# Performance work log

Hardware: AMD Instinct MI355X
Metric: run time of the kernel (lower is better)

The kernel has to match this reference:

```python
import jax, jax.numpy as jnp
import numpy as np

N, D_IN, H, L, K, Q = 131072, 384, 256, 32, 512, 4


def _lin_init(key, fan_in, fan_out):
    s = 1.0 / np.sqrt(fan_in)
    kw, kb = jax.random.split(key)
    w = jax.random.uniform(kw, (fan_in, fan_out), minval=-s, maxval=s, dtype=jnp.float32)
    b = jax.random.uniform(kb, (fan_out,), minval=-s, maxval=s, dtype=jnp.float32)
    return w, b


def setup_inputs() -> dict:
    key = jax.random.key(0)
    ks = jax.random.split(key, 8)
    enc_w1, enc_b1 = _lin_init(ks[1], D_IN, H)
    enc_w2, enc_b2 = _lin_init(ks[2], H, H)
    enc_w3, enc_b3 = _lin_init(ks[3], H, L)
    dec_w1, dec_b1 = _lin_init(ks[4], L, H)
    dec_w2, dec_b2 = _lin_init(ks[5], H, H)
    dec_w3, dec_b3 = _lin_init(ks[6], H, D_IN)
    codebooks = jax.random.normal(ks[7], (Q, K, L), dtype=jnp.float32) * 0.02
    x = jax.random.normal(ks[0], (N, D_IN), dtype=jnp.float32)
    return dict(x=x,
                enc_w1=enc_w1, enc_b1=enc_b1, enc_w2=enc_w2, enc_b2=enc_b2,
                enc_w3=enc_w3, enc_b3=enc_b3,
                dec_w1=dec_w1, dec_b1=dec_b1, dec_w2=dec_w2, dec_b2=dec_b2,
                dec_w3=dec_w3, dec_b3=dec_b3,
                codebooks=codebooks)


def _encoder(x, w1, b1, w2, b2, w3, b3):
    h = jax.nn.relu(x @ w1 + b1)
    h = jax.nn.relu(h @ w2 + b2)
    return h @ w3 + b3


def _decoder(z, w1, b1, w2, b2, w3, b3):
    h = jax.nn.relu(z @ w1 + b1)
    h = jax.nn.relu(h @ w2 + b2)
    return h @ w3 + b3


def _residual_vq(z, codebooks):
    """Residual VQ: Q stages of nearest-codeword lookup on the running residual.
    Returns (z_quantized with straight-through, indices [N,Q], commitment loss)."""
    residual = z
    quant_sum = jnp.zeros_like(z)
    indices = []
    commit = jnp.float32(0.0)
    for q in range(codebooks.shape[0]):  # small fixed loop over quantizer stages
        cb = codebooks[q]  # [K, L]
        # squared L2 distances [N, K] via expansion (cdist + argmin)
        d = (jnp.sum(residual * residual, axis=-1, keepdims=True)
             - 2.0 * residual @ cb.T
             + jnp.sum(cb * cb, axis=-1))
        idx = jnp.argmin(d, axis=-1)          # [N]
        qv = cb[idx]                          # gather [N, L]
        commit = commit + jnp.mean((jax.lax.stop_gradient(qv) - residual) ** 2)
        quant_sum = quant_sum + qv
        residual = residual - jax.lax.stop_gradient(qv)
        indices.append(idx)
    # straight-through estimator
    z_q = z + jax.lax.stop_gradient(quant_sum - z)
    return z_q, jnp.stack(indices, axis=-1), commit


def reference(x, enc_w1, enc_b1, enc_w2, enc_b2, enc_w3, enc_b3,
              dec_w1, dec_b1, dec_w2, dec_b2, dec_w3, dec_b3, codebooks):
    z = _encoder(x, enc_w1, enc_b1, enc_w2, enc_b2, enc_w3, enc_b3)
    z_q, indices, commit = _residual_vq(z, codebooks)
    x_recon = _decoder(z_q, dec_w1, dec_b1, dec_w2, dec_b2, dec_w3, dec_b3)
    return x_recon, indices, commit
```

## Files before the change

### kernel.cpp

```cpp
#include <hip/hip_runtime.h>
#include <hip/hip_bf16.h>
#include <math.h>


#define N_ROWS 131072
#define D_IN   384
#define H_DIM  256
#define L_DIM  32
#define K_CB   512
#define Q_ST   4
#define VQ_RPB 128
#define NPART  (N_ROWS / VQ_RPB)

typedef __attribute__((ext_vector_type(8))) short short8v;
typedef __attribute__((ext_vector_type(4))) float f32x4;

__device__ __forceinline__ ushort f2bf(float v)
{
    __hip_bfloat16 b = __float2bfloat16(v);
    return *reinterpret_cast<ushort*>(&b);
}

__device__ __forceinline__ float np_sumsq32(const float* __restrict__ v)
{
    #pragma clang fp contract(off)
    float s0 = v[0]*v[0], s1 = v[1]*v[1], s2 = v[2]*v[2], s3 = v[3]*v[3];
    float s4 = v[4]*v[4], s5 = v[5]*v[5], s6 = v[6]*v[6], s7 = v[7]*v[7];
    s0 = s0 + v[8]*v[8];   s1 = s1 + v[9]*v[9];   s2 = s2 + v[10]*v[10]; s3 = s3 + v[11]*v[11];
    s4 = s4 + v[12]*v[12]; s5 = s5 + v[13]*v[13]; s6 = s6 + v[14]*v[14]; s7 = s7 + v[15]*v[15];
    s0 = s0 + v[16]*v[16]; s1 = s1 + v[17]*v[17]; s2 = s2 + v[18]*v[18]; s3 = s3 + v[19]*v[19];
    s4 = s4 + v[20]*v[20]; s5 = s5 + v[21]*v[21]; s6 = s6 + v[22]*v[22]; s7 = s7 + v[23]*v[23];
    s0 = s0 + v[24]*v[24]; s1 = s1 + v[25]*v[25]; s2 = s2 + v[26]*v[26]; s3 = s3 + v[27]*v[27];
    s4 = s4 + v[28]*v[28]; s5 = s5 + v[29]*v[29]; s6 = s6 + v[30]*v[30]; s7 = s7 + v[31]*v[31];
    return ((s0 + s1) + (s2 + s3)) + ((s4 + s5) + (s6 + s7));
}

template<bool RELU>
__global__ __launch_bounds__(256, 2)
void gemm_bias(const float* __restrict__ A, const float* __restrict__ B,
               const float* __restrict__ bias, float* __restrict__ C,
               int K)
{
    #pragma clang fp contract(off)
    __shared__ float As2[32][133];
    __shared__ float Bs[32][256];
    const int t  = threadIdx.x;
    const int tc = t & 15;
    const int tr = t >> 4;
    const size_t row0 = (size_t)blockIdx.x * 128;

    float acc[8][16];
    #pragma unroll
    for (int i = 0; i < 8; ++i)
        #pragma unroll
        for (int j = 0; j < 16; ++j) acc[i][j] = 0.f;

    const int ar = t >> 3, ak = (t & 7) << 2;
    const int brow = t >> 6, bcol = (t & 63) << 2;

    for (int k0 = 0; k0 < K; k0 += 32) {
        #pragma unroll
        for (int i = 0; i < 4; ++i) {
            int r = ar + (i << 5);
            float4 v = *reinterpret_cast<const float4*>(A + (row0 + r) * (size_t)K + k0 + ak);
            As2[ak + 0][r] = v.x; As2[ak + 1][r] = v.y;
            As2[ak + 2][r] = v.z; As2[ak + 3][r] = v.w;
        }
        #pragma unroll
        for (int i = 0; i < 8; ++i) {
            int rb = brow + (i << 2);
            float4 v = *reinterpret_cast<const float4*>(B + (size_t)(k0 + rb) * H_DIM + bcol);
            *reinterpret_cast<float4*>(&Bs[rb][bcol]) = v;
        }
        __syncthreads();
        #pragma unroll
        for (int k = 0; k < 32; ++k) {
            float a[8], b[16];
            *reinterpret_cast<float4*>(&a[0]) = *reinterpret_cast<const float4*>(&As2[k][tr << 3]);
            *reinterpret_cast<float4*>(&a[4]) = *reinterpret_cast<const float4*>(&As2[k][(tr << 3) + 4]);
            #pragma unroll
            for (int g = 0; g < 4; ++g)
                *reinterpret_cast<float4*>(&b[g << 2]) =
                    *reinterpret_cast<const float4*>(&Bs[k][(g << 6) + (tc << 2)]);
            #pragma unroll
            for (int i = 0; i < 8; ++i)
                #pragma unroll
                for (int j = 0; j < 16; ++j) acc[i][j] = fmaf(a[i], b[j], acc[i][j]);
        }
        __syncthreads();
    }

    #pragma unroll
    for (int i = 0; i < 8; ++i) {
        size_t r = row0 + (tr << 3) + i;
        #pragma unroll
        for (int g = 0; g < 4; ++g) {
            int c = (g << 6) + (tc << 2);
            float v[4];
            #pragma unroll
            for (int j = 0; j < 4; ++j) {
                float u = acc[i][(g << 2) + j] + bias[c + j];
                if (RELU) u = fmaxf(u, 0.0f);
                v[j] = u;
            }
            *reinterpret_cast<float4*>(C + r * H_DIM + c) = *reinterpret_cast<float4*>(&v[0]);
        }
    }
}

__global__ __launch_bounds__(256)
void gemm_z(const float* __restrict__ A, const float* __restrict__ W,
            const float* __restrict__ bv, float* __restrict__ Z)
{
    #pragma clang fp contract(off)
    __shared__ float As2[32][133];
    __shared__ float Ws[32][36];
    const int t = threadIdx.x;
    const int cgz = t & 7, rgz = t >> 3;
    const size_t row0 = (size_t)blockIdx.x * 128;

    float acc[4][4];
    #pragma unroll
    for (int i = 0; i < 4; ++i)
        #pragma unroll
        for (int j = 0; j < 4; ++j) acc[i][j] = 0.f;

    const int ar = t >> 3, ak = (t & 7) << 2;
    for (int k0 = 0; k0 < H_DIM; k0 += 32) {
        #pragma unroll
        for (int i = 0; i < 4; ++i) {
            int r = ar + (i << 5);
            float4 v = *reinterpret_cast<const float4*>(A + (row0 + r) * (size_t)H_DIM + k0 + ak);
            As2[ak + 0][r] = v.x; As2[ak + 1][r] = v.y;
            As2[ak + 2][r] = v.z; As2[ak + 3][r] = v.w;
        }
        {
            int kr = t >> 3, cc = (t & 7) << 2;
            float4 v = *reinterpret_cast<const float4*>(W + (size_t)(k0 + kr) * L_DIM + cc);
            *reinterpret_cast<float4*>(&Ws[kr][cc]) = v;
        }
        __syncthreads();
        #pragma unroll
        for (int k = 0; k < 32; ++k) {
            float a[4], w[4];
            *reinterpret_cast<float4*>(&a[0]) = *reinterpret_cast<const float4*>(&As2[k][rgz << 2]);
            *reinterpret_cast<float4*>(&w[0]) = *reinterpret_cast<const float4*>(&Ws[k][cgz << 2]);
            #pragma unroll
            for (int i = 0; i < 4; ++i)
                #pragma unroll
                for (int j = 0; j < 4; ++j) acc[i][j] = fmaf(a[i], w[j], acc[i][j]);
        }
        __syncthreads();
    }
    #pragma unroll
    for (int i = 0; i < 4; ++i) {
        size_t row = row0 + (rgz << 2) + i;
        float v[4];
        #pragma unroll
        for (int j = 0; j < 4; ++j) v[j] = acc[i][j] + bv[(cgz << 2) + j];
        *reinterpret_cast<float4*>(Z + row * L_DIM + (cgz << 2)) = *reinterpret_cast<float4*>(&v[0]);
    }
}

__global__ __launch_bounds__(256)
void cnorm_kernel(const float* __restrict__ cbs, float* __restrict__ cnorm)
{
    #pragma clang fp contract(off)
    int g = blockIdx.x * 256 + threadIdx.x;
    const float* c = cbs + (size_t)g * L_DIM;
    float cl[L_DIM];
    #pragma unroll
    for (int l = 0; l < L_DIM; ++l) cl[l] = c[l];
    cnorm[g] = np_sumsq32(cl);
}

__global__ __launch_bounds__(256)
void prep_wt(const float* __restrict__ W, ushort* __restrict__ Wt, int K, int N)
{
    int g = blockIdx.x * 256 + threadIdx.x;
    if (g >= K * N) return;
    int n = g / K, k = g - n * K;
    Wt[g] = f2bf(W[(size_t)k * N + n]);
}

__global__ __launch_bounds__(256)
void vq9_kernel(const float* __restrict__ zbuf, const float* __restrict__ cbs,
                const float* __restrict__ cnorm_g, ushort* __restrict__ zqb,
                float* __restrict__ idxOut, double* __restrict__ commitPart,
                int rowBase)
{
    #pragma clang fp contract(off)
    __shared__ float  cbL[K_CB * L_DIM];
    __shared__ float  cnL[K_CB];
    __shared__ float  sd0[4][64], sd1[4][64];
    __shared__ int    si0[4][64], si1[4][64];
    __shared__ double sred[256];

    const int t = threadIdx.x;
    const int w = t >> 6;
    const int l = t & 63;
    const size_t lrow0 = (size_t)blockIdx.x * VQ_RPB + l;
    const size_t lrow1 = lrow0 + 64;
    const size_t grow0 = (size_t)rowBase + lrow0;
    const size_t grow1 = (size_t)rowBase + lrow1;
    const int c0 = w << 7;

    float r0[L_DIM], r1[L_DIM];
    {
        const float4* zp0 = reinterpret_cast<const float4*>(zbuf + lrow0 * L_DIM);
        const float4* zp1 = reinterpret_cast<const float4*>(zbuf + lrow1 * L_DIM);
        #pragma unroll
        for (int j = 0; j < 8; ++j) {
            float4 a = zp0[j], b = zp1[j];
            r0[4*j+0]=a.x; r0[4*j+1]=a.y; r0[4*j+2]=a.z; r0[4*j+3]=a.w;
            r1[4*j+0]=b.x; r1[4*j+1]=b.y; r1[4*j+2]=b.z; r1[4*j+3]=b.w;
        }
    }

    int bidx0[Q_ST], bidx1[Q_ST];
    double cAcc = 0.0;

    #pragma unroll 1
    for (int q = 0; q < Q_ST; ++q) {
        __syncthreads();
        {
            const float4* src = reinterpret_cast<const float4*>(cbs + (size_t)q * K_CB * L_DIM);
            float4* dst = reinterpret_cast<float4*>(cbL);
            #pragma unroll
            for (int i = 0; i < 16; ++i) dst[t + (i << 8)] = src[t + (i << 8)];
            cnL[t]       = cnorm_g[q * K_CB + t];
            cnL[t + 256] = cnorm_g[q * K_CB + t + 256];
        }
        __syncthreads();

        float rr0 = np_sumsq32(r0);
        float rr1 = np_sumsq32(r1);
        float bd0 = __builtin_inff(), bd1 = __builtin_inff();
        int   bi0 = c0, bi1 = c0;

        #pragma unroll 1
        for (int cc = 0; cc < 128; cc += 2) {
            const int c = c0 + cc;
            const float4* w0 = reinterpret_cast<const float4*>(cbL + (c << 5));
            const float4* w1 = w0 + 8;
            float a00 = 0.f, a01 = 0.f, a10 = 0.f, a11 = 0.f;
            #pragma unroll
            for (int j = 0; j < 8; ++j) {
                float4 u = w0[j], v = w1[j];
                a00 = fmaf(r0[4*j+0], u.x, a00);  a01 = fmaf(r0[4*j+0], v.x, a01);
                a10 = fmaf(r1[4*j+0], u.x, a10);  a11 = fmaf(r1[4*j+0], v.x, a11);
                a00 = fmaf(r0[4*j+1], u.y, a00);  a01 = fmaf(r0[4*j+1], v.y, a01);
                a10 = fmaf(r1[4*j+1], u.y, a10);  a11 = fmaf(r1[4*j+1], v.y, a11);
                a00 = fmaf(r0[4*j+2], u.z, a00);  a01 = fmaf(r0[4*j+2], v.z, a01);
                a10 = fmaf(r1[4*j+2], u.z, a10);  a11 = fmaf(r1[4*j+2], v.z, a11);
                a00 = fmaf(r0[4*j+3], u.w, a00);  a01 = fmaf(r0[4*j+3], v.w, a01);
                a10 = fmaf(r1[4*j+3], u.w, a10);  a11 = fmaf(r1[4*j+3], v.w, a11);
            }
            float cn0 = cnL[c], cn1 = cnL[c + 1];
            float d00 = (rr0 - 2.0f * a00) + cn0;
            float d01 = (rr0 - 2.0f * a01) + cn1;
            float d10 = (rr1 - 2.0f * a10) + cn0;
            float d11 = (rr1 - 2.0f * a11) + cn1;
            if (d00 < bd0) { bd0 = d00; bi0 = c; }
            if (d01 < bd0) { bd0 = d01; bi0 = c + 1; }
            if (d10 < bd1) { bd1 = d10; bi1 = c; }
            if (d11 < bd1) { bd1 = d11; bi1 = c + 1; }
        }

        sd0[w][l] = bd0; si0[w][l] = bi0;
        sd1[w][l] = bd1; si1[w][l] = bi1;
        __syncthreads();

        float g0 = sd0[0][l]; int gi0 = si0[0][l];
        float g1 = sd1[0][l]; int gi1 = si1[0][l];
        #pragma unroll
        for (int ww = 1; ww < 4; ++ww) {
            float od = sd0[ww][l]; int oi = si0[ww][l];
            if (od < g0 || (od == g0 && oi < gi0)) { g0 = od; gi0 = oi; }
            od = sd1[ww][l]; oi = si1[ww][l];
            if (od < g1 || (od == g1 && oi < gi1)) { g1 = od; gi1 = oi; }
        }
        bidx0[q] = gi0;
        bidx1[q] = gi1;

        {
            const float4* p0 = reinterpret_cast<const float4*>(cbL + (gi0 << 5));
            const float4* p1 = reinterpret_cast<const float4*>(cbL + (gi1 << 5));
            float cs0 = 0.f, cs1 = 0.f;
            #pragma unroll
            for (int j = 0; j < 8; ++j) {
                float4 v0 = p0[j], v1 = p1[j];
                float df;
                df = v0.x - r0[4*j+0]; cs0 = fmaf(df, df, cs0); r0[4*j+0] = r0[4*j+0] - v0.x;
                df = v0.y - r0[4*j+1]; cs0 = fmaf(df, df, cs0); r0[4*j+1] = r0[4*j+1] - v0.y;
                df = v0.z - r0[4*j+2]; cs0 = fmaf(df, df, cs0); r0[4*j+2] = r0[4*j+2] - v0.z;
                df = v0.w - r0[4*j+3]; cs0 = fmaf(df, df, cs0); r0[4*j+3] = r0[4*j+3] - v0.w;
                df = v1.x - r1[4*j+0]; cs1 = fmaf(df, df, cs1); r1[4*j+0] = r1[4*j+0] - v1.x;
                df = v1.y - r1[4*j+1]; cs1 = fmaf(df, df, cs1); r1[4*j+1] = r1[4*j+1] - v1.y;
                df = v1.z - r1[4*j+2]; cs1 = fmaf(df, df, cs1); r1[4*j+2] = r1[4*j+2] - v1.z;
                df = v1.w - r1[4*j+3]; cs1 = fmaf(df, df, cs1); r1[4*j+3] = r1[4*j+3] - v1.w;
            }
            if (w == 0) { cAcc += (double)cs0; cAcc += (double)cs1; }
        }
    }

    if (w == 0) {
        float4 iv0 = make_float4((float)bidx0[0], (float)bidx0[1], (float)bidx0[2], (float)bidx0[3]);
        float4 iv1 = make_float4((float)bidx1[0], (float)bidx1[1], (float)bidx1[2], (float)bidx1[3]);
        *reinterpret_cast<float4*>(idxOut + grow0 * Q_ST) = iv0;
        *reinterpret_cast<float4*>(idxOut + grow1 * Q_ST) = iv1;

        const float4* zp0 = reinterpret_cast<const float4*>(zbuf + lrow0 * L_DIM);
        const float4* zp1 = reinterpret_cast<const float4*>(zbuf + lrow1 * L_DIM);
        ushort zq0[L_DIM], zq1[L_DIM];
        #pragma unroll
        for (int j = 0; j < 8; ++j) {
            float4 a = zp0[j], b = zp1[j];
            zq0[4*j+0] = f2bf(a.x - r0[4*j+0]);
            zq0[4*j+1] = f2bf(a.y - r0[4*j+1]);
            zq0[4*j+2] = f2bf(a.z - r0[4*j+2]);
            zq0[4*j+3] = f2bf(a.w - r0[4*j+3]);
            zq1[4*j+0] = f2bf(b.x - r1[4*j+0]);
            zq1[4*j+1] = f2bf(b.y - r1[4*j+1]);
            zq1[4*j+2] = f2bf(b.z - r1[4*j+2]);
            zq1[4*j+3] = f2bf(b.w - r1[4*j+3]);
        }
        uint4* o0 = reinterpret_cast<uint4*>(zqb + lrow0 * L_DIM);
        uint4* o1 = reinterpret_cast<uint4*>(zqb + lrow1 * L_DIM);
        const uint4* s0 = reinterpret_cast<const uint4*>(zq0);
        const uint4* s1 = reinterpret_cast<const uint4*>(zq1);
        #pragma unroll
        for (int j = 0; j < 4; ++j) { o0[j] = s0[j]; o1[j] = s1[j]; }
    }

    sred[t] = (w == 0) ? cAcc : 0.0;
    __syncthreads();
    for (int s = 128; s > 0; s >>= 1) {
        if (t < s) sred[t] += sred[t + s];
        __syncthreads();
    }
    if (t == 0) commitPart[rowBase / VQ_RPB + blockIdx.x] = sred[0];
}

template<bool RELU, bool OUTBF16>
__global__ __launch_bounds__(256)
void mfma_gemm(const ushort* __restrict__ A, const ushort* __restrict__ Bt,
               const float* __restrict__ bias, void* __restrict__ Cout,
               int K, int Nout)
{
    __shared__ ushort As[128][40];
    __shared__ ushort Bs[128][40];
    const int t    = threadIdx.x;
    const int lane = t & 63;
    const int wid  = t >> 6;
    const int wr = wid >> 1, wc = wid & 1;
    const size_t row0 = (size_t)blockIdx.x * 128;
    const int    col0 = blockIdx.y * 128;

    f32x4 acc[4][4] = {};
    const int srow = t >> 1;
    const int sh   = (t & 1) << 4;

    for (int k0 = 0; k0 < K; k0 += 32) {
        {
            const ushort* ap = A + (row0 + srow) * (size_t)K + k0 + sh;
            uint4 v0 = *reinterpret_cast<const uint4*>(ap);
            uint4 v1 = *reinterpret_cast<const uint4*>(ap + 8);
            *reinterpret_cast<uint4*>(&As[srow][sh])     = v0;
            *reinterpret_cast<uint4*>(&As[srow][sh + 8]) = v1;
            const ushort* bp = Bt + (size_t)(col0 + srow) * K + k0 + sh;
            uint4 w0 = *reinterpret_cast<const uint4*>(bp);
            uint4 w1 = *reinterpret_cast<const uint4*>(bp + 8);
            *reinterpret_cast<uint4*>(&Bs[srow][sh])     = w0;
            *reinterpret_cast<uint4*>(&Bs[srow][sh + 8]) = w1;
        }
        __syncthreads();
        const int l15 = lane & 15, lk = (lane >> 4) << 3;
        short8v af[4], bf[4];
        #pragma unroll
        for (int f = 0; f < 4; ++f) {
            af[f] = *reinterpret_cast<const short8v*>(&As[(wr << 6) + (f << 4) + l15][lk]);
            bf[f] = *reinterpret_cast<const short8v*>(&Bs[(wc << 6) + (f << 4) + l15][lk]);
        }
        #pragma unroll
        for (int i = 0; i < 4; ++i)
            #pragma unroll
            for (int j = 0; j < 4; ++j)
                acc[i][j] = __builtin_amdgcn_mfma_f32_16x16x32_bf16(af[i], bf[j], acc[i][j], 0, 0, 0);
        __syncthreads();
    }

    const int l15 = lane & 15, lr4 = (lane >> 4) << 2;
    #pragma unroll
    for (int i = 0; i < 4; ++i) {
        #pragma unroll
        for (int j = 0; j < 4; ++j) {
            int col = col0 + (wc << 6) + (j << 4) + l15;
            float bv = bias[col];
            #pragma unroll
            for (int rj = 0; rj < 4; ++rj) {
                size_t row = row0 + (wr << 6) + (i << 4) + lr4 + rj;
                float v = acc[i][j][rj] + bv;
                if (RELU) v = fmaxf(v, 0.f);
                if (OUTBF16)
                    reinterpret_cast<ushort*>(Cout)[row * Nout + col] = f2bf(v);
                else
                    reinterpret_cast<float*>(Cout)[row * Nout + col] = v;
            }
        }
    }
}

__global__ __launch_bounds__(256)
void commit_finalize(const double* __restrict__ commitPart, float* __restrict__ outCommit)
{
    __shared__ double sred[256];
    const int t = threadIdx.x;
    double s = 0.0;
    for (int i = t; i < NPART; i += 256) s += commitPart[i];
    sred[t] = s;
    __syncthreads();
    for (int st = 128; st > 0; st >>= 1) {
        if (t < st) sred[t] += sred[t + st];
        __syncthreads();
    }
    if (t == 0)
        outCommit[0] = (float)(sred[0] / ((double)N_ROWS * (double)L_DIM));
}

extern "C" void kernel_launch(void* const* d_in, const int* in_sizes, int n_in,
                              void* d_out, int out_size, void* d_ws, size_t ws_size,
                              hipStream_t stream)
{
    const float* x      = (const float*)d_in[0];
    const float* enc_w1 = (const float*)d_in[1];
    const float* enc_b1 = (const float*)d_in[2];
    const float* enc_w2 = (const float*)d_in[3];
    const float* enc_b2 = (const float*)d_in[4];
    const float* enc_w3 = (const float*)d_in[5];
    const float* enc_b3 = (const float*)d_in[6];
    const float* dec_w1 = (const float*)d_in[7];
    const float* dec_b1 = (const float*)d_in[8];
    const float* dec_w2 = (const float*)d_in[9];
    const float* dec_b2 = (const float*)d_in[10];
    const float* dec_w3 = (const float*)d_in[11];
    const float* dec_b3 = (const float*)d_in[12];
    const float* cbs    = (const float*)d_in[13];

    float* out       = (float*)d_out;
    float* xrec      = out;
    float* idxOut    = out + (size_t)N_ROWS * D_IN;
    float* commitOut = idxOut + (size_t)N_ROWS * Q_ST;

    char*   wsb        = (char*)d_ws;
    float*  cnorm      = (float*)wsb;
    double* commitPart = (double*)(wsb + 8192);
    ushort* w1t        = (ushort*)(wsb + 16384);
    ushort* w2t        = (ushort*)(wsb + 32768);
    ushort* w3t        = (ushort*)(wsb + 163840);
    char*   bufs       = wsb + 360448;

    size_t availB = (ws_size > 360448) ? ws_size - 360448 : 0;
    long long chunk = (long long)(availB / 3264);
    chunk = (chunk / 256) * 256;
    if (chunk > N_ROWS) chunk = N_ROWS;
    if (chunk < 256) chunk = 256;

    float*  zbuf = (float*)bufs;
    float*  bufA = zbuf + (size_t)chunk * L_DIM;
    float*  bufB = bufA + (size_t)chunk * H_DIM;
    ushort* zqb  = (ushort*)(bufB + (size_t)chunk * H_DIM);
    ushort* h1b  = zqb + (size_t)chunk * L_DIM;
    ushort* h2b  = h1b + (size_t)chunk * H_DIM;

    cnorm_kernel<<<8, 256, 0, stream>>>(cbs, cnorm);
    prep_wt<<<(L_DIM  * H_DIM + 255) / 256, 256, 0, stream>>>(dec_w1, w1t, L_DIM, H_DIM);
    prep_wt<<<(H_DIM * H_DIM + 255) / 256, 256, 0, stream>>>(dec_w2, w2t, H_DIM, H_DIM);
    prep_wt<<<(H_DIM * D_IN + 255) / 256, 256, 0, stream>>>(dec_w3, w3t, H_DIM, D_IN);

    for (long long ro = 0; ro < N_ROWS; ro += chunk) {
        long long R = N_ROWS - ro;
        if (R > chunk) R = chunk;
        unsigned g1 = (unsigned)(R / 128);
        dim3 g2(g1, 2);
        dim3 g3(g1, 3);
        gemm_bias<true><<<g1, 256, 0, stream>>>(x + ro * D_IN, enc_w1, enc_b1, bufA, D_IN);
        gemm_bias<true><<<g1, 256, 0, stream>>>(bufA, enc_w2, enc_b2, bufB, H_DIM);
        gemm_z<<<g1, 256, 0, stream>>>(bufB, enc_w3, enc_b3, zbuf);
        vq9_kernel<<<(unsigned)(R / VQ_RPB), 256, 0, stream>>>(zbuf, cbs, cnorm, zqb,
                                                               idxOut, commitPart, (int)ro);
        mfma_gemm<true,  true ><<<g2, 256, 0, stream>>>(zqb, w1t, dec_b1, h1b, L_DIM, H_DIM);
        mfma_gemm<true,  true ><<<g2, 256, 0, stream>>>(h1b, w2t, dec_b2, h2b, H_DIM, H_DIM);
        mfma_gemm<false, false><<<g3, 256, 0, stream>>>(h2b, w3t, dec_b3, xrec + ro * D_IN, H_DIM, D_IN);
    }

    commit_finalize<<<1, 256, 0, stream>>>(commitPart, commitOut);
}
```

Measured before the change: 919.3 us.

## Restructure encoder fp32 GEMM to read B via wave-uniform scalar loads

Replaces the encoder fp32 GEMM's shared-memory B tile with wave-uniform reads straight from global memory. Each wave owns 64 output columns and each lane owns two rows, so B values can be fetched with scalar loads and broadcast, cutting LDS traffic and one staging step. The cost is 128 accumulators per thread, which raises register pressure and lowers occupancy, and B reads now rely on the scalar cache instead of LDS. The A tile is still staged transposed in LDS.

```diff
diff --git a/kernel.cpp b/kernel.cpp
--- a/kernel.cpp
+++ b/kernel.cpp
@@ -36,27 +36,24 @@
 }
 
 template<bool RELU>
-__global__ __launch_bounds__(256, 2)
-void gemm_bias(const float* __restrict__ A, const float* __restrict__ B,
-               const float* __restrict__ bias, float* __restrict__ C,
-               int K)
+__global__ __launch_bounds__(256)
+void gemm_sb(const float* __restrict__ A, const float* __restrict__ B,
+             const float* __restrict__ bias, float* __restrict__ C,
+             int K)
 {
     #pragma clang fp contract(off)
     __shared__ float As2[32][133];
-    __shared__ float Bs[32][256];
-    const int t  = threadIdx.x;
-    const int tc = t & 15;
-    const int tr = t >> 4;
+    const int t = threadIdx.x;
+    const int l = t & 63;
+    const int w = __builtin_amdgcn_readfirstlane(t >> 6);
+    const int cbase = w << 6;
     const size_t row0 = (size_t)blockIdx.x * 128;
 
-    float acc[8][16];
-    #pragma unroll
-    for (int i = 0; i < 8; ++i)
-        #pragma unroll
-        for (int j = 0; j < 16; ++j) acc[i][j] = 0.f;
+    float acc0[64], acc1[64];
+    #pragma unroll
+    for (int j = 0; j < 64; ++j) { acc0[j] = 0.f; acc1[j] = 0.f; }
 
     const int ar = t >> 3, ak = (t & 7) << 2;
-    const int brow = t >> 6, bcol = (t & 63) << 2;
 
     for (int k0 = 0; k0 < K; k0 += 32) {
         #pragma unroll
@@ -66,45 +63,37 @@
             As2[ak + 0][r] = v.x; As2[ak + 1][r] = v.y;
             As2[ak + 2][r] = v.z; As2[ak + 3][r] = v.w;
         }
-        #pragma unroll
-        for (int i = 0; i < 8; ++i) {
-            int rb = brow + (i << 2);
-            float4 v = *reinterpret_cast<const float4*>(B + (size_t)(k0 + rb) * H_DIM + bcol);
-            *reinterpret_cast<float4*>(&Bs[rb][bcol]) = v;
-        }
-        __syncthreads();
-        #pragma unroll
+        __syncthreads();
+        #pragma unroll 2
         for (int k = 0; k < 32; ++k) {
-            float a[8], b[16];
-            *reinterpret_cast<float4*>(&a[0]) = *reinterpret_cast<const float4*>(&As2[k][tr << 3]);
-            *reinterpret_cast<float4*>(&a[4]) = *reinterpret_cast<const float4*>(&As2[k][(tr << 3) + 4]);
-            #pragma unroll
-            for (int g = 0; g < 4; ++g)
-                *reinterpret_cast<float4*>(&b[g << 2]) =
-                    *reinterpret_cast<const float4*>(&Bs[k][(g << 6) + (tc << 2)]);
-            #pragma unroll
-            for (int i = 0; i < 8; ++i)
-                #pragma unroll
-                for (int j = 0; j < 16; ++j) acc[i][j] = fmaf(a[i], b[j], acc[i][j]);
-        }
-        __syncthreads();
-    }
-
-    #pragma unroll
-    for (int i = 0; i < 8; ++i) {
-        size_t r = row0 + (tr << 3) + i;
-        #pragma unroll
-        for (int g = 0; g < 4; ++g) {
-            int c = (g << 6) + (tc << 2);
-            float v[4];
-            #pragma unroll
-            for (int j = 0; j < 4; ++j) {
-                float u = acc[i][(g << 2) + j] + bias[c + j];
-                if (RELU) u = fmaxf(u, 0.0f);
-                v[j] = u;
+            float a0 = As2[k][l];
+            float a1 = As2[k][l + 64];
+            const float* __restrict__ Brow = B + (size_t)(k0 + k) * H_DIM + cbase;
+            #pragma unroll
+            for (int j = 0; j < 64; ++j) {
+                float bv = Brow[j];
+                acc0[j] = fmaf(a0, bv, acc0[j]);
+                acc1[j] = fmaf(a1, bv, acc1[j]);
             }
-            *reinterpret_cast<float4*>(C + r * H_DIM + c) = *reinterpret_cast<float4*>(&v[0]);
-        }
+        }
+        __syncthreads();
+    }
+
+    float* C0 = C + (row0 + l) * (size_t)H_DIM + cbase;
+    float* C1 = C + (row0 + l + 64) * (size_t)H_DIM + cbase;
+    #pragma unroll
+    for (int g = 0; g < 16; ++g) {
+        float v0[4], v1[4];
+        #pragma unroll
+        for (int j = 0; j < 4; ++j) {
+            float bv = bias[cbase + (g << 2) + j];
+            float u0 = acc0[(g << 2) + j] + bv;
+            float u1 = acc1[(g << 2) + j] + bv;
+            if (RELU) { u0 = fmaxf(u0, 0.0f); u1 = fmaxf(u1, 0.0f); }
+            v0[j] = u0; v1[j] = u1;
+        }
+        *reinterpret_cast<float4*>(C0 + (g << 2)) = *reinterpret_cast<float4*>(&v0[0]);
+        *reinterpret_cast<float4*>(C1 + (g << 2)) = *reinterpret_cast<float4*>(&v1[0]);
     }
 }
 
@@ -484,8 +473,8 @@
         unsigned g1 = (unsigned)(R / 128);
         dim3 g2(g1, 2);
         dim3 g3(g1, 3);
-        gemm_bias<true><<<g1, 256, 0, stream>>>(x + ro * D_IN, enc_w1, enc_b1, bufA, D_IN);
-        gemm_bias<true><<<g1, 256, 0, stream>>>(bufA, enc_w2, enc_b2, bufB, H_DIM);
+        gemm_sb<true><<<g1, 256, 0, stream>>>(x + ro * D_IN, enc_w1, enc_b1, bufA, D_IN);
+        gemm_sb<true><<<g1, 256, 0, stream>>>(bufA, enc_w2, enc_b2, bufB, H_DIM);
         gemm_z<<<g1, 256, 0, stream>>>(bufB, enc_w3, enc_b3, zbuf);
         vq9_kernel<<<(unsigned)(R / VQ_RPB), 256, 0, stream>>>(zbuf, cbs, cnorm, zqb,
                                                                idxOut, commitPart, (int)ro);
```

New measurement: 1.227 ms. 33.5% more time.
